# Kernel tuning notes

Hardware: AMD Instinct MI355X
Metric: run time of the kernel (lower is better)

The kernel has to match this reference:

```python
import jax, jax.numpy as jnp
import numpy as np

H = 8          # num_heads
EPS = 1e-5     # nn.LayerNorm default eps


def _attn(x, kv, wq, bq, wk, bk, wv, bv, wo, bo):
    # x: [B, Nq, D] queries; kv: [B, Nk, D] keys/values. softmax over keys (dim=-1).
    B, Nq, D = x.shape
    Nk = kv.shape[1]
    d = D // H
    q = (x @ wq + bq).reshape(B, Nq, H, d).transpose(0, 2, 1, 3)   # [B,h,Nq,d]
    k = (kv @ wk + bk).reshape(B, Nk, H, d).transpose(0, 2, 1, 3)  # [B,h,Nk,d]
    v = (kv @ wv + bv).reshape(B, Nk, H, d).transpose(0, 2, 1, 3)  # [B,h,Nk,d]
    scores = jnp.einsum('bhqd,bhkd->bhqk', q, k) * (d ** -0.5)
    a = jax.nn.softmax(scores, axis=-1)                            # softmax_dim='keys'
    ctx = jnp.einsum('bhqk,bhkd->bhqd', a, v)
    ctx = ctx.transpose(0, 2, 1, 3).reshape(B, Nq, D)
    return ctx @ wo + bo


def _ln(x, g, b):
    mu = jnp.mean(x, axis=-1, keepdims=True)
    var = jnp.var(x, axis=-1, keepdims=True)  # biased, matches torch LayerNorm
    return (x - mu) * jax.lax.rsqrt(var + EPS) * g + b


def setup_inputs() -> dict:
    key = jax.random.key(0)
    B, Nq, Nk, D = 2, 2048, 4096, 512
    Hid = 4 * D
    ks = jax.random.split(key, 32)
    s = 0.02
    r = lambda i, shp: jax.random.normal(ks[i], shp, dtype=jnp.float32) * s
    inp = {
        'x': jax.random.normal(ks[0], (B, Nq, D), dtype=jnp.float32),
        'cross': jax.random.normal(ks[1], (B, Nk, D), dtype=jnp.float32),
        # cross-attention projections (stored as [in, out])
        'ca_wq': r(2, (D, D)), 'ca_bq': jnp.zeros((D,), jnp.float32),
        'ca_wk': r(3, (D, D)), 'ca_bk': jnp.zeros((D,), jnp.float32),
        'ca_wv': r(4, (D, D)), 'ca_bv': jnp.zeros((D,), jnp.float32),
        'ca_wo': r(5, (D, D)), 'ca_bo': jnp.zeros((D,), jnp.float32),
        # self-attention projections
        'sa_wq': r(6, (D, D)), 'sa_bq': jnp.zeros((D,), jnp.float32),
        'sa_wk': r(7, (D, D)), 'sa_bk': jnp.zeros((D,), jnp.float32),
        'sa_wv': r(8, (D, D)), 'sa_bv': jnp.zeros((D,), jnp.float32),
        'sa_wo': r(9, (D, D)), 'sa_bo': jnp.zeros((D,), jnp.float32),
        # layer norms
        'ln1_g': jnp.ones((D,), jnp.float32), 'ln1_b': jnp.zeros((D,), jnp.float32),
        'ln2_g': jnp.ones((D,), jnp.float32), 'ln2_b': jnp.zeros((D,), jnp.float32),
        # MLP
        'mlp_w1': r(10, (D, Hid)), 'mlp_b1': jnp.zeros((Hid,), jnp.float32),
        'mlp_w2': r(11, (Hid, D)), 'mlp_b2': jnp.zeros((D,), jnp.float32),
    }
    return inp


def reference(x, cross,
              ca_wq, ca_bq, ca_wk, ca_bk, ca_wv, ca_bv, ca_wo, ca_bo,
              sa_wq, sa_bq, sa_wk, sa_bk, sa_wv, sa_bv, sa_wo, sa_bo,
              ln1_g, ln1_b, ln2_g, ln2_b,
              mlp_w1, mlp_b1, mlp_w2, mlp_b2):
    # a) cross-attention
    xc = _attn(x, cross, ca_wq, ca_bq, ca_wk, ca_bk, ca_wv, ca_bv, ca_wo, ca_bo)
    # b,c) LN then self-attention (Q=K=V=ln1(xc))
    xn = _ln(xc, ln1_g, ln1_b)
    xs = _attn(xn, xn, sa_wq, sa_bq, sa_wk, sa_bk, sa_wv, sa_bv, sa_wo, sa_bo)
    # d) residual
    y = xc + xs
    # e,f) LN + GELU MLP (torch GELU default = exact erf)
    h1 = jax.nn.gelu(_ln(y, ln2_g, ln2_b) @ mlp_w1 + mlp_b1, approximate=False)
    z = h1 @ mlp_w2 + mlp_b2
    # g) residual
    return y + z
```

## Files before the change

### kernel.cpp

```cpp
#include <hip/hip_runtime.h>
#include <math.h>

typedef _Float16 f16;
typedef __attribute__((ext_vector_type(8))) _Float16 f16x8;
typedef __attribute__((ext_vector_type(4))) _Float16 f16x4;
typedef __attribute__((ext_vector_type(4))) float f32x4;
typedef __attribute__((ext_vector_type(16))) float f32x16;
typedef __attribute__((ext_vector_type(2))) __fp16 h16x2;

#define QSCALE 0.1803368801111204f

__device__ __forceinline__ void gl_lds16(const f16* g, f16* l) {
    __builtin_amdgcn_global_load_lds((const __attribute__((address_space(1))) void*)g,
                                     (__attribute__((address_space(3))) void*)l, 16, 0, 0);
}

struct PrepArgs {
    const float* ws[10]; f16* wd[10];
    const float* x; f16* xh;
    const float* cross; f16* ch;
};
__global__ __launch_bounds__(256)
void prep_all(PrepArgs p) {
    __shared__ float t[32][33];
    int bid = blockIdx.x, tid = threadIdx.x;
    if (bid < 4096) {
        const float* W; f16* Wt; int K, N, nx, ky;
        if (bid < 2048) {
            int wi = bid >> 8, tl = bid & 255;
            W = p.ws[wi]; Wt = p.wd[wi]; K = 512; N = 512; nx = tl & 15; ky = tl >> 4;
        } else if (bid < 3072) {
            int tl = bid - 2048;
            W = p.ws[8]; Wt = p.wd[8]; K = 512; N = 2048; nx = tl & 63; ky = tl >> 6;
        } else {
            int tl = bid - 3072;
            W = p.ws[9]; Wt = p.wd[9]; K = 2048; N = 512; nx = tl & 15; ky = tl >> 4;
        }
        int tx = tid & 31, ty = tid >> 5;
        int n0 = nx * 32, k0 = ky * 32;
#pragma unroll
        for (int i = 0; i < 4; i++)
            t[ty + i * 8][tx] = W[(size_t)(k0 + ty + i * 8) * N + n0 + tx];
        __syncthreads();
#pragma unroll
        for (int i = 0; i < 4; i++)
            Wt[(size_t)(n0 + ty + i * 8) * K + k0 + tx] = (f16)t[tx][ty + i * 8];
    } else {
        const float* X; f16* Y; size_t cb;
        if (bid < 6144) { X = p.x; Y = p.xh; cb = bid - 4096; }
        else            { X = p.cross; Y = p.ch; cb = bid - 6144; }
        size_t i = (cb * 256 + tid) * 4;
        f32x4 v = *(const f32x4*)(X + i);
        f16x4 o;
        o[0] = (f16)v[0]; o[1] = (f16)v[1]; o[2] = (f16)v[2]; o[3] = (f16)v[3];
        *(f16x4*)(Y + i) = o;
    }
}

__global__ __launch_bounds__(128)
void layernorm_f16(const float* __restrict__ X, const float* __restrict__ g,
                   const float* __restrict__ bta, f16* __restrict__ Y)
{
    __shared__ float red[4];
    int row = blockIdx.x;
    int tid = threadIdx.x;
    const float* x = X + (size_t)row * 512;
    f32x4 v = *(const f32x4*)(x + tid * 4);
    float s  = v[0] + v[1] + v[2] + v[3];
    float ss = v[0] * v[0] + v[1] * v[1] + v[2] * v[2] + v[3] * v[3];
#pragma unroll
    for (int m = 1; m < 64; m <<= 1) {
        s  += __shfl_xor(s, m, 64);
        ss += __shfl_xor(ss, m, 64);
    }
    int wave = tid >> 6, lane = tid & 63;
    if (lane == 0) { red[wave * 2] = s; red[wave * 2 + 1] = ss; }
    __syncthreads();
    s = red[0] + red[2]; ss = red[1] + red[3];
    float mu  = s * (1.0f / 512);
    float var = ss * (1.0f / 512) - mu * mu;
    float inv = rsqrtf(var + 1e-5f);
    f32x4 gv = *(const f32x4*)(g + tid * 4);
    f32x4 bv = *(const f32x4*)(bta + tid * 4);
    f16x4 o;
#pragma unroll
    for (int i = 0; i < 4; i++) o[i] = (f16)((v[i] - mu) * inv * gv[i] + bv[i]);
    *(f16x4*)(Y + (size_t)row * 512 + tid * 4) = o;
}

__global__ __launch_bounds__(256)
void gemm_f16(const f16* __restrict__ A, const f16* __restrict__ Wt,
              const float* __restrict__ b0, const float* __restrict__ b1,
              const float* __restrict__ b2, const float* __restrict__ res,
              float* __restrict__ Cf32, f16* __restrict__ C16,
              f16* __restrict__ hm0, f16* __restrict__ hm1, f16* __restrict__ hm2,
              f16* __restrict__ vtp, int vseg,
              int N, int K, int NBshift, int fused, int act, float s0)
{
    __shared__ __align__(16) f16 As[2][128 * 64];
    __shared__ __align__(16) f16 Bs[2][128 * 64];
    int tid = threadIdx.x, lane = tid & 63, wave = tid >> 6;
    int quad = lane >> 4, ln16 = lane & 15;
    int wm = wave >> 1, wn = wave & 1;
    int bm0 = blockIdx.y * 128, bn0 = blockIdx.x * 128;

    f32x4 acc[4][4];
#pragma unroll
    for (int i = 0; i < 4; i++)
#pragma unroll
        for (int j = 0; j < 4; j++) acc[i][j] = (f32x4){0.f, 0.f, 0.f, 0.f};

    const f16* ag[4]; const f16* bg[4]; int Loff[4];
#pragma unroll
    for (int j = 0; j < 4; j++) {
        int L = tid + j * 256;
        int row = L >> 3, cc = (L & 7) ^ (row & 7);
        ag[j] = A  + (size_t)(bm0 + row) * K + cc * 8;
        bg[j] = Wt + (size_t)(bn0 + row) * K + cc * 8;
        Loff[j] = L * 8;
    }
    int sw0 = (quad ^ (ln16 & 7)) * 8, sw1 = ((4 + quad) ^ (ln16 & 7)) * 8;

#pragma unroll
    for (int j = 0; j < 4; j++) { gl_lds16(ag[j], &As[0][Loff[j]]); gl_lds16(bg[j], &Bs[0][Loff[j]]); }
#pragma unroll
    for (int j = 0; j < 4; j++) { ag[j] += 64; bg[j] += 64; }

    int cur = 0;
    for (int kt = 0; kt < K; kt += 64) {
        __syncthreads();
        if (kt + 64 < K) {
            int nxt = cur ^ 1;
#pragma unroll
            for (int j = 0; j < 4; j++) { gl_lds16(ag[j], &As[nxt][Loff[j]]); gl_lds16(bg[j], &Bs[nxt][Loff[j]]); }
#pragma unroll
            for (int j = 0; j < 4; j++) { ag[j] += 64; bg[j] += 64; }
        }
        const f16* Ac = As[cur]; const f16* Bc = Bs[cur];
#pragma unroll
        for (int h = 0; h < 2; h++) {
            int sw = h ? sw1 : sw0;
            f16x8 af[4], bf[4];
#pragma unroll
            for (int mt = 0; mt < 4; mt++)
                af[mt] = *(const f16x8*)&Ac[(wm * 64 + mt * 16 + ln16) * 64 + sw];
#pragma unroll
            for (int nt = 0; nt < 4; nt++)
                bf[nt] = *(const f16x8*)&Bc[(wn * 64 + nt * 16 + ln16) * 64 + sw];
#pragma unroll
            for (int mt = 0; mt < 4; mt++)
#pragma unroll
                for (int nt = 0; nt < 4; nt++)
                    acc[mt][nt] = __builtin_amdgcn_mfma_f32_16x16x32_f16(af[mt], bf[nt], acc[mt][nt], 0, 0, 0);
        }
        cur ^= 1;
    }

    int NB = 1 << NBshift;
#pragma unroll
    for (int mt = 0; mt < 4; mt++) {
#pragma unroll
        for (int nt = 0; nt < 4; nt++) {
            int row = bm0 + wm * 64 + mt * 16 + quad * 4;
            int col = bn0 + wn * 64 + nt * 16 + ln16;
            float bv;
            if (fused) {
                int seg = col >> 9;
                const float* bp = seg == 0 ? b0 : (seg == 1 ? b1 : b2);
                bv = bp[col & 511];
            } else bv = b0[col];
            int seg = col >> 9;
            if (vtp && seg == vseg) {
                int hh = (col >> 6) & 7, d = col & 63;
                int bt = row >> NBshift, rr = row & (NB - 1);
                f16x4 o4;
#pragma unroll
                for (int i = 0; i < 4; i++) o4[i] = (f16)(acc[mt][nt][i] + bv);
                *(f16x4*)&vtp[(((size_t)bt * 8 + hh) * 64 + d) * NB + rr] = o4;
            } else {
#pragma unroll
                for (int i = 0; i < 4; i++) {
                    int r = row + i;
                    float v = acc[mt][nt][i] + bv;
                    size_t idx = (size_t)r * N + col;
                    if (res) v += res[idx];
                    if (act) v = 0.5f * v * (1.0f + erff(v * 0.70710678118654752f));
                    if (Cf32) Cf32[idx] = v;
                    if (C16) C16[idx] = (f16)v;
                    if (hm0) {
                        f16* hp = seg == 0 ? hm0 : (seg == 1 ? hm1 : hm2);
                        float vv = seg == 0 ? v * s0 : v;
                        int hh = (col >> 6) & 7, d = col & 63;
                        int bt = r >> NBshift, rr = r & (NB - 1);
                        hp[(((size_t)bt * 8 + hh) * NB + rr) * 64 + d] = (f16)vv;
                    }
                }
            }
        }
    }
}

__global__ __launch_bounds__(256)
void gemm64(const f16* __restrict__ A, const f16* __restrict__ Wt,
            const float* __restrict__ bias, const float* __restrict__ res,
            float* __restrict__ Cf32, f16* __restrict__ hm0,
            int N, int K, int NBshift, float s0)
{
    __shared__ __align__(16) f16 As[2][64 * 64];
    __shared__ __align__(16) f16 Bs[2][64 * 64];
    int tid = threadIdx.x, lane = tid & 63, wave = tid >> 6;
    int quad = lane >> 4, ln16 = lane & 15;
    int wm = wave >> 1, wn = wave & 1;
    int bm0 = blockIdx.y * 64, bn0 = blockIdx.x * 64;

    f32x4 acc[2][2];
#pragma unroll
    for (int i = 0; i < 2; i++)
#pragma unroll
        for (int j = 0; j < 2; j++) acc[i][j] = (f32x4){0.f, 0.f, 0.f, 0.f};

    const f16* ag[2]; const f16* bg[2]; int Loff[2];
#pragma unroll
    for (int j = 0; j < 2; j++) {
        int L = tid + j * 256;
        int row = L >> 3, cc = (L & 7) ^ (row & 7);
        ag[j] = A  + (size_t)(bm0 + row) * K + cc * 8;
        bg[j] = Wt + (size_t)(bn0 + row) * K + cc * 8;
        Loff[j] = L * 8;
    }
    int sw0 = (quad ^ (ln16 & 7)) * 8, sw1 = ((4 + quad) ^ (ln16 & 7)) * 8;

#pragma unroll
    for (int j = 0; j < 2; j++) { gl_lds16(ag[j], &As[0][Loff[j]]); gl_lds16(bg[j], &Bs[0][Loff[j]]); }
#pragma unroll
    for (int j = 0; j < 2; j++) { ag[j] += 64; bg[j] += 64; }

    int cur = 0;
    for (int kt = 0; kt < K; kt += 64) {
        __syncthreads();
        if (kt + 64 < K) {
            int nxt = cur ^ 1;
#pragma unroll
            for (int j = 0; j < 2; j++) { gl_lds16(ag[j], &As[nxt][Loff[j]]); gl_lds16(bg[j], &Bs[nxt][Loff[j]]); }
#pragma unroll
            for (int j = 0; j < 2; j++) { ag[j] += 64; bg[j] += 64; }
        }
        const f16* Ac = As[cur]; const f16* Bc = Bs[cur];
#pragma unroll
        for (int h = 0; h < 2; h++) {
            int sw = h ? sw1 : sw0;
            f16x8 af[2], bf[2];
#pragma unroll
            for (int mt = 0; mt < 2; mt++)
                af[mt] = *(const f16x8*)&Ac[(wm * 32 + mt * 16 + ln16) * 64 + sw];
#pragma unroll
            for (int nt = 0; nt < 2; nt++)
                bf[nt] = *(const f16x8*)&Bc[(wn * 32 + nt * 16 + ln16) * 64 + sw];
#pragma unroll
            for (int mt = 0; mt < 2; mt++)
#pragma unroll
                for (int nt = 0; nt < 2; nt++)
                    acc[mt][nt] = __builtin_amdgcn_mfma_f32_16x16x32_f16(af[mt], bf[nt], acc[mt][nt], 0, 0, 0);
        }
        cur ^= 1;
    }

    int NB = 1 << NBshift;
#pragma unroll
    for (int mt = 0; mt < 2; mt++) {
#pragma unroll
        for (int nt = 0; nt < 2; nt++) {
            int row = bm0 + wm * 32 + mt * 16 + quad * 4;
            int col = bn0 + wn * 32 + nt * 16 + ln16;
            float bv = bias[col];
#pragma unroll
            for (int i = 0; i < 4; i++) {
                int r = row + i;
                float v = acc[mt][nt][i] + bv;
                size_t idx = (size_t)r * N + col;
                if (res) v += res[idx];
                if (Cf32) Cf32[idx] = v;
                if (hm0) {
                    int hh = (col >> 6) & 7, d = col & 63;
                    int bt = r >> NBshift, rr = r & (NB - 1);
                    hm0[(((size_t)bt * 8 + hh) * NB + rr) * 64 + d] = (f16)(v * s0);
                }
            }
        }
    }
}

__global__ __launch_bounds__(512, 4)
void attention_split(const f16* __restrict__ Qh, const f16* __restrict__ Kh,
                     const f16* __restrict__ Vt, f16* __restrict__ Op,
                     float* __restrict__ Lsum, int Nk, int nsp_log)
{
    __shared__ __align__(16) f16 Kt[2][64 * 64];
    __shared__ __align__(16) f16 Vs[2][64 * 64];
    int z = blockIdx.z, b = z >> nsp_log, sp = z & ((1 << nsp_log) - 1);
    int h8 = blockIdx.y, bh = b * 8 + h8;
    int Nkh = Nk >> nsp_log;
    int tid = threadIdx.x, lane = tid & 63, wave = tid >> 6;
    int lq = lane & 31, hh = lane >> 5, l7 = lane & 7;
    int qrow0 = blockIdx.x * 256 + wave * 32;

    f16x8 qf[4];
#pragma unroll
    for (int s = 0; s < 4; s++)
        qf[s] = *(const f16x8*)(Qh + ((size_t)bh * 2048 + qrow0 + lq) * 64 + s * 16 + hh * 8);

    f32x16 oacc[2];
#pragma unroll
    for (int db = 0; db < 2; db++)
#pragma unroll
        for (int r = 0; r < 16; r++) oacc[db][r] = 0.f;
    float lacc = 0.f;

    const f16* kb = Kh + ((size_t)bh * Nk + sp * Nkh) * 64;
    const f16* vb = Vt + (size_t)bh * 64 * Nk + sp * Nkh;

    const f16* kg; const f16* vg; int Lo;
    {
        int L = tid;
        int row = L >> 3, cc = (L & 7) ^ (row & 7);
        kg = kb + (size_t)row * 64 + cc * 8;
        vg = vb + (size_t)row * Nk + cc * 8;
        Lo = L * 8;
    }

    int off[2][4];
#pragma unroll
    for (int g = 0; g < 2; g++)
#pragma unroll
        for (int s = 0; s < 4; s++)
            off[g][s] = (g * 32 + lq) * 64 + (((2 * s + hh) ^ l7) * 8);

    gl_lds16(kg, &Kt[0][Lo]);
    gl_lds16(vg, &Vs[0][Lo]);
    kg += 64 * 64; vg += 64;

    int cur = 0;
    for (int kt = 0; kt < Nkh; kt += 64) {
        __syncthreads();
        if (kt + 64 < Nkh) {
            int nxt = cur ^ 1;
            gl_lds16(kg, &Kt[nxt][Lo]);
            gl_lds16(vg, &Vs[nxt][Lo]);
            kg += 64 * 64; vg += 64;
        }
        const f16* Ktc = Kt[cur]; const f16* Vsc = Vs[cur];

#pragma unroll
        for (int kbk = 0; kbk < 2; kbk++) {
            f32x16 c;
#pragma unroll
            for (int r = 0; r < 16; r++) c[r] = 0.f;
#pragma unroll
            for (int s = 0; s < 4; s++) {
                f16x8 kf = *(const f16x8*)&Ktc[off[kbk][s]];
                c = __builtin_amdgcn_mfma_f32_32x32x16_f16(kf, qf[s], c, 0, 0, 0);
            }
            int pr[8];
#pragma unroll
            for (int m = 0; m < 8; m++) {
                float e0 = exp2f(c[2 * m]), e1 = exp2f(c[2 * m + 1]);
                lacc += e0 + e1;
                union { h16x2 h; int i; } u;
                u.h = __builtin_amdgcn_cvt_pkrtz(e0, e1);
                pr[m] = u.i;
            }
#pragma unroll
            for (int t = 0; t < 2; t++) {
                int p0 = pr[4 * t + 0], p1 = pr[4 * t + 1];
                int p2 = pr[4 * t + 2], p3 = pr[4 * t + 3];
                int s0 = __shfl_xor(p0, 32, 64);
                int s1 = __shfl_xor(p1, 32, 64);
                int s2 = __shfl_xor(p2, 32, 64);
                int s3 = __shfl_xor(p3, 32, 64);
                union { int i[4]; f16x8 v; } bu;
                bu.i[0] = hh ? s2 : p0;
                bu.i[1] = hh ? s3 : p1;
                bu.i[2] = hh ? p2 : s0;
                bu.i[3] = hh ? p3 : s1;
                int ks = kbk * 2 + t;
#pragma unroll
                for (int db = 0; db < 2; db++) {
                    f16x8 vf = *(const f16x8*)&Vsc[off[db][ks]];
                    oacc[db] = __builtin_amdgcn_mfma_f32_32x32x16_f16(vf, bu.v, oacc[db], 0, 0, 0);
                }
            }
        }
        cur ^= 1;
    }

    float ltot = lacc + __shfl_xor(lacc, 32, 64);
    size_t rowb = ((size_t)(sp * 16 + bh) * 2048 + qrow0 + lq) * 64;
#pragma unroll
    for (int db = 0; db < 2; db++)
#pragma unroll
        for (int rq = 0; rq < 4; rq++) {
            f16x4 o4;
#pragma unroll
            for (int i = 0; i < 4; i++) o4[i] = (f16)oacc[db][rq * 4 + i];
            *(f16x4*)&Op[rowb + db * 32 + rq * 8 + hh * 4] = o4;
        }
    if (hh == 0)
        Lsum[(size_t)(sp * 16 + bh) * 2048 + qrow0 + lq] = ltot;
}

__global__ __launch_bounds__(256)
void attn_combine(const f16* __restrict__ Op, const float* __restrict__ Lsum,
                  f16* __restrict__ O, int nsplit)
{
    int t = blockIdx.x * 256 + threadIdx.x;
    int d = t & 63;
    int q = (t >> 6) & 2047;
    int bh = t >> 17;
    int b = bh >> 3, h = bh & 7;
    float l = 0.f, val = 0.f;
#pragma unroll 4
    for (int s = 0; s < nsplit; s++) {
        l   += Lsum[(size_t)(s * 16 + bh) * 2048 + q];
        val += (float)Op[((size_t)(s * 16 + bh) * 2048 + q) * 64 + d];
    }
    O[((size_t)b * 2048 + q) * 512 + h * 64 + d] = (f16)(val / l);
}

extern "C" void kernel_launch(void* const* d_in, const int* in_sizes, int n_in,
                              void* d_out, int out_size, void* d_ws, size_t ws_size,
                              hipStream_t stream)
{
    (void)in_sizes; (void)n_in; (void)out_size; (void)ws_size;
    const float* x      = (const float*)d_in[0];
    const float* cross  = (const float*)d_in[1];
    const float* ca_wq  = (const float*)d_in[2];
    const float* ca_bq  = (const float*)d_in[3];
    const float* ca_wk  = (const float*)d_in[4];
    const float* ca_bk  = (const float*)d_in[5];
    const float* ca_wv  = (const float*)d_in[6];
    const float* ca_bv  = (const float*)d_in[7];
    const float* ca_wo  = (const float*)d_in[8];
    const float* ca_bo  = (const float*)d_in[9];
    const float* sa_wq  = (const float*)d_in[10];
    const float* sa_bq  = (const float*)d_in[11];
    const float* sa_wk  = (const float*)d_in[12];
    const float* sa_bk  = (const float*)d_in[13];
    const float* sa_wv  = (const float*)d_in[14];
    const float* sa_bv  = (const float*)d_in[15];
    const float* sa_wo  = (const float*)d_in[16];
    const float* sa_bo  = (const float*)d_in[17];
    const float* ln1_g  = (const float*)d_in[18];
    const float* ln1_b  = (const float*)d_in[19];
    const float* ln2_g  = (const float*)d_in[20];
    const float* ln2_b  = (const float*)d_in[21];
    const float* mlp_w1 = (const float*)d_in[22];
    const float* mlp_b1 = (const float*)d_in[23];
    const float* mlp_w2 = (const float*)d_in[24];
    const float* mlp_b2 = (const float*)d_in[25];
    float* out = (float*)d_out;

    float* XC = (float*)d_ws;
    float* Yb = XC + 2097152;
    f16* fb   = (f16*)(Yb + 2097152);
    f16* xh     = fb;
    f16* crossh = xh + 2097152;
    f16* xnh    = crossh + 4194304;
    f16* xn2h   = xnh + 2097152;
    f16* Qh     = xn2h + 2097152;
    f16* Kh     = Qh + 2097152;
    f16* Vh     = Kh + 4194304;
    f16* Vtb    = Vh + 4194304;
    f16* ctxh   = Vtb + 4194304;
    f16* h1h    = ctxh + 2097152;
    f16* t_caq  = h1h + 8388608;
    f16* t_cak  = t_caq + 262144;
    f16* t_cav  = t_cak + 262144;
    f16* t_cao  = t_cav + 262144;
    f16* t_saq  = t_cao + 262144;
    f16* t_sak  = t_saq + 262144;
    f16* t_sav  = t_sak + 262144;
    f16* t_sao  = t_sav + 262144;
    f16* t_w1   = t_sao + 262144;
    f16* t_w2   = t_w1 + 1048576;
    float* Lsum = (float*)(t_w2 + 1048576);

    PrepArgs pa;
    pa.ws[0] = ca_wq; pa.wd[0] = t_caq;
    pa.ws[1] = ca_wk; pa.wd[1] = t_cak;
    pa.ws[2] = ca_wv; pa.wd[2] = t_cav;
    pa.ws[3] = ca_wo; pa.wd[3] = t_cao;
    pa.ws[4] = sa_wq; pa.wd[4] = t_saq;
    pa.ws[5] = sa_wk; pa.wd[5] = t_sak;
    pa.ws[6] = sa_wv; pa.wd[6] = t_sav;
    pa.ws[7] = sa_wo; pa.wd[7] = t_sao;
    pa.ws[8] = mlp_w1; pa.wd[8] = t_w1;
    pa.ws[9] = mlp_w2; pa.wd[9] = t_w2;
    pa.x = x; pa.xh = xh; pa.cross = cross; pa.ch = crossh;
    prep_all<<<10240, 256, 0, stream>>>(pa);

    gemm64<<<dim3(8, 64), 256, 0, stream>>>(xh, t_caq, ca_bq, nullptr, nullptr, Qh,
                                            512, 512, 11, QSCALE);
    gemm_f16<<<dim3(8, 64), 256, 0, stream>>>(crossh, t_cak, ca_bk, ca_bv, nullptr, nullptr,
        nullptr, nullptr, Kh, nullptr, nullptr, Vtb, 1, 1024, 512, 12, 1, 0, 1.0f);
    attention_split<<<dim3(8, 8, 8), 512, 0, stream>>>(Qh, Kh, Vtb, h1h, Lsum, 4096, 2);
    attn_combine<<<8192, 256, 0, stream>>>(h1h, Lsum, ctxh, 4);
    gemm64<<<dim3(8, 64), 256, 0, stream>>>(ctxh, t_cao, ca_bo, nullptr, XC, nullptr,
                                            512, 512, 11, 1.0f);
    layernorm_f16<<<4096, 128, 0, stream>>>(XC, ln1_g, ln1_b, xnh);
    gemm_f16<<<dim3(12, 32), 256, 0, stream>>>(xnh, t_saq, sa_bq, sa_bk, sa_bv, nullptr,
        nullptr, nullptr, Qh, Kh, nullptr, Vtb, 2, 1536, 512, 11, 1, 0, QSCALE);
    attention_split<<<dim3(8, 8, 8), 512, 0, stream>>>(Qh, Kh, Vtb, h1h, Lsum, 2048, 2);
    attn_combine<<<8192, 256, 0, stream>>>(h1h, Lsum, ctxh, 4);
    gemm64<<<dim3(8, 64), 256, 0, stream>>>(ctxh, t_sao, sa_bo, XC, Yb, nullptr,
                                            512, 512, 11, 1.0f);
    layernorm_f16<<<4096, 128, 0, stream>>>(Yb, ln2_g, ln2_b, xn2h);
    gemm_f16<<<dim3(16, 32), 256, 0, stream>>>(xn2h, t_w1, mlp_b1, nullptr, nullptr, nullptr,
        nullptr, h1h, nullptr, nullptr, nullptr, nullptr, 0, 2048, 512, 11, 0, 1, 1.0f);
    gemm64<<<dim3(8, 64), 256, 0, stream>>>(h1h, t_w2, mlp_b2, Yb, out, nullptr,
                                            512, 2048, 11, 1.0f);
}
```

Baseline: 364.5 us.

## Split-K the final MLP GEMM with atomic accumulation; prefill residual in layernorm

The last MLP down-projection (K=2048) now runs as a 4-way split-K gemm_f16 launch that atomically adds partial sums into the output, with the residual plus bias written beforehand by the second layernorm kernel. This raises the block count for a GEMM that otherwise had few long-running blocks. The attention kernel also switches to the raw hardware exp2 builtin and spreads the row-sum accumulation over four partial accumulators to shorten the dependency chain. Atomics add contention, nondeterministic summation order and extra global traffic.

```diff
diff --git a/kernel.cpp b/kernel.cpp
--- a/kernel.cpp
+++ b/kernel.cpp
@@ -59,7 +59,8 @@
 
 __global__ __launch_bounds__(128)
 void layernorm_f16(const float* __restrict__ X, const float* __restrict__ g,
-                   const float* __restrict__ bta, f16* __restrict__ Y)
+                   const float* __restrict__ bta, f16* __restrict__ Y,
+                   const float* __restrict__ addb, float* __restrict__ outpre)
 {
     __shared__ float red[4];
     int row = blockIdx.x;
@@ -86,6 +87,13 @@
 #pragma unroll
     for (int i = 0; i < 4; i++) o[i] = (f16)((v[i] - mu) * inv * gv[i] + bv[i]);
     *(f16x4*)(Y + (size_t)row * 512 + tid * 4) = o;
+    if (outpre) {
+        f32x4 ab = *(const f32x4*)(addb + tid * 4);
+        f32x4 pv;
+#pragma unroll
+        for (int i = 0; i < 4; i++) pv[i] = v[i] + ab[i];
+        *(f32x4*)(outpre + (size_t)row * 512 + tid * 4) = pv;
+    }
 }
 
 __global__ __launch_bounds__(256)
@@ -95,7 +103,8 @@
               float* __restrict__ Cf32, f16* __restrict__ C16,
               f16* __restrict__ hm0, f16* __restrict__ hm1, f16* __restrict__ hm2,
               f16* __restrict__ vtp, int vseg,
-              int N, int K, int NBshift, int fused, int act, float s0)
+              int N, int K, int Kstride, int NBshift, int fused, int act,
+              int katomic, float s0)
 {
     __shared__ __align__(16) f16 As[2][128 * 64];
     __shared__ __align__(16) f16 Bs[2][128 * 64];
@@ -103,6 +112,7 @@
     int quad = lane >> 4, ln16 = lane & 15;
     int wm = wave >> 1, wn = wave & 1;
     int bm0 = blockIdx.y * 128, bn0 = blockIdx.x * 128;
+    int kz = blockIdx.z * K;
 
     f32x4 acc[4][4];
 #pragma unroll
@@ -115,8 +125,8 @@
     for (int j = 0; j < 4; j++) {
         int L = tid + j * 256;
         int row = L >> 3, cc = (L & 7) ^ (row & 7);
-        ag[j] = A  + (size_t)(bm0 + row) * K + cc * 8;
-        bg[j] = Wt + (size_t)(bn0 + row) * K + cc * 8;
+        ag[j] = A  + (size_t)(bm0 + row) * Kstride + kz + cc * 8;
+        bg[j] = Wt + (size_t)(bn0 + row) * Kstride + kz + cc * 8;
         Loff[j] = L * 8;
     }
     int sw0 = (quad ^ (ln16 & 7)) * 8, sw1 = ((4 + quad) ^ (ln16 & 7)) * 8;
@@ -163,6 +173,12 @@
         for (int nt = 0; nt < 4; nt++) {
             int row = bm0 + wm * 64 + mt * 16 + quad * 4;
             int col = bn0 + wn * 64 + nt * 16 + ln16;
+            if (katomic) {
+#pragma unroll
+                for (int i = 0; i < 4; i++)
+                    atomicAdd(&Cf32[(size_t)(row + i) * N + col], acc[mt][nt][i]);
+                continue;
+            }
             float bv;
             if (fused) {
                 int seg = col >> 9;
@@ -314,7 +330,7 @@
     for (int db = 0; db < 2; db++)
 #pragma unroll
         for (int r = 0; r < 16; r++) oacc[db][r] = 0.f;
-    float lacc = 0.f;
+    float la[4] = {0.f, 0.f, 0.f, 0.f};
 
     const f16* kb = Kh + ((size_t)bh * Nk + sp * Nkh) * 64;
     const f16* vb = Vt + (size_t)bh * 64 * Nk + sp * Nkh;
@@ -363,8 +379,10 @@
             int pr[8];
 #pragma unroll
             for (int m = 0; m < 8; m++) {
-                float e0 = exp2f(c[2 * m]), e1 = exp2f(c[2 * m + 1]);
-                lacc += e0 + e1;
+                float e0 = __builtin_amdgcn_exp2f(c[2 * m]);
+                float e1 = __builtin_amdgcn_exp2f(c[2 * m + 1]);
+                la[2 * (m & 1)]     += e0;
+                la[2 * (m & 1) + 1] += e1;
                 union { h16x2 h; int i; } u;
                 u.h = __builtin_amdgcn_cvt_pkrtz(e0, e1);
                 pr[m] = u.i;
@@ -393,6 +411,7 @@
         cur ^= 1;
     }
 
+    float lacc = (la[0] + la[1]) + (la[2] + la[3]);
     float ltot = lacc + __shfl_xor(lacc, 32, 64);
     size_t rowb = ((size_t)(sp * 16 + bh) * 2048 + qrow0 + lq) * 64;
 #pragma unroll
@@ -501,21 +520,21 @@
     gemm64<<<dim3(8, 64), 256, 0, stream>>>(xh, t_caq, ca_bq, nullptr, nullptr, Qh,
                                             512, 512, 11, QSCALE);
     gemm_f16<<<dim3(8, 64), 256, 0, stream>>>(crossh, t_cak, ca_bk, ca_bv, nullptr, nullptr,
-        nullptr, nullptr, Kh, nullptr, nullptr, Vtb, 1, 1024, 512, 12, 1, 0, 1.0f);
+        nullptr, nullptr, Kh, nullptr, nullptr, Vtb, 1, 1024, 512, 512, 12, 1, 0, 0, 1.0f);
     attention_split<<<dim3(8, 8, 8), 512, 0, stream>>>(Qh, Kh, Vtb, h1h, Lsum, 4096, 2);
     attn_combine<<<8192, 256, 0, stream>>>(h1h, Lsum, ctxh, 4);
     gemm64<<<dim3(8, 64), 256, 0, stream>>>(ctxh, t_cao, ca_bo, nullptr, XC, nullptr,
                                             512, 512, 11, 1.0f);
-    layernorm_f16<<<4096, 128, 0, stream>>>(XC, ln1_g, ln1_b, xnh);
+    layernorm_f16<<<4096, 128, 0, stream>>>(XC, ln1_g, ln1_b, xnh, nullptr, nullptr);
     gemm_f16<<<dim3(12, 32), 256, 0, stream>>>(xnh, t_saq, sa_bq, sa_bk, sa_bv, nullptr,
-        nullptr, nullptr, Qh, Kh, nullptr, Vtb, 2, 1536, 512, 11, 1, 0, QSCALE);
+        nullptr, nullptr, Qh, Kh, nullptr, Vtb, 2, 1536, 512, 512, 11, 1, 0, 0, QSCALE);
     attention_split<<<dim3(8, 8, 8), 512, 0, stream>>>(Qh, Kh, Vtb, h1h, Lsum, 2048, 2);
     attn_combine<<<8192, 256, 0, stream>>>(h1h, Lsum, ctxh, 4);
     gemm64<<<dim3(8, 64), 256, 0, stream>>>(ctxh, t_sao, sa_bo, XC, Yb, nullptr,
                                             512, 512, 11, 1.0f);
-    layernorm_f16<<<4096, 128, 0, stream>>>(Yb, ln2_g, ln2_b, xn2h);
+    layernorm_f16<<<4096, 128, 0, stream>>>(Yb, ln2_g, ln2_b, xn2h, mlp_b2, out);
     gemm_f16<<<dim3(16, 32), 256, 0, stream>>>(xn2h, t_w1, mlp_b1, nullptr, nullptr, nullptr,
-        nullptr, h1h, nullptr, nullptr, nullptr, nullptr, 0, 2048, 512, 11, 0, 1, 1.0f);
-    gemm64<<<dim3(8, 64), 256, 0, stream>>>(h1h, t_w2, mlp_b2, Yb, out, nullptr,
-                                            512, 2048, 11, 1.0f);
-}
+        nullptr, h1h, nullptr, nullptr, nullptr, nullptr, 0, 2048, 512, 512, 11, 0, 1, 0, 1.0f);
+    gemm_f16<<<dim3(4, 32, 4), 256, 0, stream>>>(h1h, t_w2, nullptr, nullptr, nullptr, nullptr,
+        out, nullptr, nullptr, nullptr, nullptr, nullptr, 0, 512, 512, 2048, 11, 0, 0, 1, 1.0f);
+}
```

Result: no change. 363.7 us (-0.2%).

## Double attention key tile to 128 and use raw exp2 with split row-sum accumulators

Applied to the files above, without the earlier changes.

The split attention kernel now processes 128 keys per iteration instead of 64, with two async global-to-LDS loads per thread per buffer. This halves the number of barriers and loop iterations. It also switches to the hardware exp2 intrinsic and spreads the softmax row sum over four accumulators to shorten dependency chains. In exchange, LDS use doubles to 64KB per block, which can limit how many blocks fit per CU under the launch bound of 4, and the wider V rows use an XOR swizzle only over the low 3 bits, which may cause bank conflicts.

```diff
diff --git a/kernel.cpp b/kernel.cpp
--- a/kernel.cpp
+++ b/kernel.cpp
@@ -295,8 +295,8 @@
                      const f16* __restrict__ Vt, f16* __restrict__ Op,
                      float* __restrict__ Lsum, int Nk, int nsp_log)
 {
-    __shared__ __align__(16) f16 Kt[2][64 * 64];
-    __shared__ __align__(16) f16 Vs[2][64 * 64];
+    __shared__ __align__(16) f16 Kt[2][128 * 64];
+    __shared__ __align__(16) f16 Vs[2][64 * 128];
     int z = blockIdx.z, b = z >> nsp_log, sp = z & ((1 << nsp_log) - 1);
     int h8 = blockIdx.y, bh = b * 8 + h8;
     int Nkh = Nk >> nsp_log;
@@ -314,57 +314,71 @@
     for (int db = 0; db < 2; db++)
 #pragma unroll
         for (int r = 0; r < 16; r++) oacc[db][r] = 0.f;
-    float lacc = 0.f;
+    float la[4] = {0.f, 0.f, 0.f, 0.f};
 
     const f16* kb = Kh + ((size_t)bh * Nk + sp * Nkh) * 64;
     const f16* vb = Vt + (size_t)bh * 64 * Nk + sp * Nkh;
 
-    const f16* kg; const f16* vg; int Lo;
-    {
-        int L = tid;
-        int row = L >> 3, cc = (L & 7) ^ (row & 7);
-        kg = kb + (size_t)row * 64 + cc * 8;
-        vg = vb + (size_t)row * Nk + cc * 8;
-        Lo = L * 8;
-    }
-
-    int off[2][4];
-#pragma unroll
-    for (int g = 0; g < 2; g++)
-#pragma unroll
-        for (int s = 0; s < 4; s++)
-            off[g][s] = (g * 32 + lq) * 64 + (((2 * s + hh) ^ l7) * 8);
-
-    gl_lds16(kg, &Kt[0][Lo]);
-    gl_lds16(vg, &Vs[0][Lo]);
-    kg += 64 * 64; vg += 64;
+    const f16* kg[2]; const f16* vg[2]; int LoK[2], LoV[2];
+#pragma unroll
+    for (int j = 0; j < 2; j++) {
+        int L = tid + j * 512;
+        int rK = L >> 3, cK = (L & 7) ^ (rK & 7);
+        kg[j] = kb + (size_t)rK * 64 + cK * 8;
+        LoK[j] = L * 8;
+        int rV = L >> 4, cV = (L & 15) ^ (rV & 7);
+        vg[j] = vb + (size_t)rV * Nk + cV * 8;
+        LoV[j] = L * 8;
+    }
+
+    int krow[4], vrow[2], kchk[4], vchk[8];
+#pragma unroll
+    for (int kbk = 0; kbk < 4; kbk++) krow[kbk] = (kbk * 32 + lq) * 64;
+#pragma unroll
+    for (int db = 0; db < 2; db++) vrow[db] = (db * 32 + lq) * 128;
+#pragma unroll
+    for (int s = 0; s < 4; s++) kchk[s] = ((2 * s + hh) ^ l7) * 8;
+#pragma unroll
+    for (int ks = 0; ks < 8; ks++) vchk[ks] = ((2 * ks + hh) ^ l7) * 8;
+
+#pragma unroll
+    for (int j = 0; j < 2; j++) {
+        gl_lds16(kg[j], &Kt[0][LoK[j]]);
+        gl_lds16(vg[j], &Vs[0][LoV[j]]);
+        kg[j] += 128 * 64; vg[j] += 128;
+    }
 
     int cur = 0;
-    for (int kt = 0; kt < Nkh; kt += 64) {
+    for (int kt = 0; kt < Nkh; kt += 128) {
         __syncthreads();
-        if (kt + 64 < Nkh) {
+        if (kt + 128 < Nkh) {
             int nxt = cur ^ 1;
-            gl_lds16(kg, &Kt[nxt][Lo]);
-            gl_lds16(vg, &Vs[nxt][Lo]);
-            kg += 64 * 64; vg += 64;
+#pragma unroll
+            for (int j = 0; j < 2; j++) {
+                gl_lds16(kg[j], &Kt[nxt][LoK[j]]);
+                gl_lds16(vg[j], &Vs[nxt][LoV[j]]);
+                kg[j] += 128 * 64; vg[j] += 128;
+            }
         }
         const f16* Ktc = Kt[cur]; const f16* Vsc = Vs[cur];
 
 #pragma unroll
-        for (int kbk = 0; kbk < 2; kbk++) {
+        for (int kbk = 0; kbk < 4; kbk++) {
             f32x16 c;
 #pragma unroll
             for (int r = 0; r < 16; r++) c[r] = 0.f;
 #pragma unroll
             for (int s = 0; s < 4; s++) {
-                f16x8 kf = *(const f16x8*)&Ktc[off[kbk][s]];
+                f16x8 kf = *(const f16x8*)&Ktc[krow[kbk] + kchk[s]];
                 c = __builtin_amdgcn_mfma_f32_32x32x16_f16(kf, qf[s], c, 0, 0, 0);
             }
             int pr[8];
 #pragma unroll
             for (int m = 0; m < 8; m++) {
-                float e0 = exp2f(c[2 * m]), e1 = exp2f(c[2 * m + 1]);
-                lacc += e0 + e1;
+                float e0 = __builtin_amdgcn_exp2f(c[2 * m]);
+                float e1 = __builtin_amdgcn_exp2f(c[2 * m + 1]);
+                la[2 * (m & 1)]     += e0;
+                la[2 * (m & 1) + 1] += e1;
                 union { h16x2 h; int i; } u;
                 u.h = __builtin_amdgcn_cvt_pkrtz(e0, e1);
                 pr[m] = u.i;
@@ -385,7 +399,7 @@
                 int ks = kbk * 2 + t;
 #pragma unroll
                 for (int db = 0; db < 2; db++) {
-                    f16x8 vf = *(const f16x8*)&Vsc[off[db][ks]];
+                    f16x8 vf = *(const f16x8*)&Vsc[vrow[db] + vchk[ks]];
                     oacc[db] = __builtin_amdgcn_mfma_f32_32x32x16_f16(vf, bu.v, oacc[db], 0, 0, 0);
                 }
             }
@@ -393,6 +407,7 @@
         cur ^= 1;
     }
 
+    float lacc = (la[0] + la[1]) + (la[2] + la[3]);
     float ltot = lacc + __shfl_xor(lacc, 32, 64);
     size_t rowb = ((size_t)(sp * 16 + bh) * 2048 + qrow0 + lq) * 64;
 #pragma unroll
```

Measured after the change: 402.6 us. 10.5% more time.
